# Performance work log

Hardware: AMD Instinct MI355X
Metric: run time of the kernel (lower is better)

## Reference

```python
import jax, jax.numpy as jnp
import numpy as np

B = 16384          # flattened rollout batch (T*N)
F = 512            # bc_args['features_dim']
H = 256            # hidden_size
E = 8              # num_skills
OUT = 32           # dim_action * steps_action = 8 * 4
DIM_ACTION = 8     # bc_args['dim_action'] + 1; output truncated to this


def setup_inputs() -> dict:
    key = jax.random.key(0)
    ks = jax.random.split(key, 5)
    features = jax.random.normal(ks[0], (B, F), dtype=jnp.float32)
    # expert MLP params, stacked over the E skills; fan-in scaled init
    W1 = jax.random.normal(ks[1], (E, F, H), dtype=jnp.float32) / np.sqrt(F)
    b1 = jnp.zeros((E, H), dtype=jnp.float32)
    W2 = jax.random.normal(ks[2], (E, H, H), dtype=jnp.float32) / np.sqrt(H)
    b2 = jnp.zeros((E, H), dtype=jnp.float32)
    W3 = jax.random.normal(ks[3], (E, H, OUT), dtype=jnp.float32) / np.sqrt(H)
    b3 = jnp.zeros((E, OUT), dtype=jnp.float32)
    master_action = jax.random.randint(ks[4], (B,), 0, E, dtype=jnp.int64)
    return {"features": features, "W1": W1, "b1": b1, "W2": W2, "b2": b2,
            "W3": W3, "b3": b3, "master_action": master_action}


def reference(features, W1, b1, W2, b2, W3, b3, master_action):
    # Per-sample skill dispatch: sample i goes through skills[master_action[i]],
    # a Linear->ReLU->Linear->ReLU->Linear MLP, output truncated to DIM_ACTION.
    # Vectorized as: run every expert over the full batch (E is a small fixed
    # set, so a Python loop over experts is fine), then select per-sample.
    sel = master_action[:, None]                      # [B, 1]
    out = jnp.zeros((features.shape[0], DIM_ACTION), dtype=features.dtype)
    for e in range(E):
        h = jax.nn.relu(features @ W1[e] + b1[e])     # [B, H]
        h = jax.nn.relu(h @ W2[e] + b2[e])            # [B, H]
        y = (h @ W3[e] + b3[e])[:, :DIM_ACTION]       # [B, DIM_ACTION]
        out = jnp.where(sel == e, y, out)
    return out
```

## Files before the change

### kernel.cpp

```cpp
#include <hip/hip_runtime.h>

#define B_TOTAL 16384
#define F_DIM 512
#define H_DIM 256
#define E_NUM 8
#define OUT_COLS 32
#define DA 8
#define TM 32
#define HSTRIDE (H_DIM + 8)

typedef __attribute__((ext_vector_type(8))) _Float16 half8;
typedef __attribute__((ext_vector_type(4))) _Float16 half4;
typedef __attribute__((ext_vector_type(4))) float float4v;

__global__ void k_bucket(const int* __restrict__ act, int* __restrict__ counts,
                         int* __restrict__ idxbuf) {
  __shared__ int wcnt[4][E_NUM];
  __shared__ int wbase[4][E_NUM];
  int t = threadIdx.x;
  int lane = t & 63, wave = t >> 6;
  int b = blockIdx.x * 256 + t;
  int e = act[b] & 7;

  unsigned long long mymask = 0;
#pragma unroll
  for (int v = 0; v < E_NUM; ++v) {
    unsigned long long m = __ballot(e == v);
    if (lane == 0) wcnt[wave][v] = (int)__popcll(m);
    if (e == v) mymask = m;
  }
  int rank = (int)__popcll(mymask & ((1ull << lane) - 1ull));
  __syncthreads();
  if (t < E_NUM) {
    int c0 = wcnt[0][t], c1 = wcnt[1][t], c2 = wcnt[2][t], c3 = wcnt[3][t];
    int base = atomicAdd(&counts[t], c0 + c1 + c2 + c3);
    wbase[0][t] = base;
    wbase[1][t] = base + c0;
    wbase[2][t] = base + c0 + c1;
    wbase[3][t] = base + c0 + c1 + c2;
  }
  __syncthreads();
  idxbuf[e * B_TOTAL + wbase[wave][e] + rank] = b;
}

__global__ void k_prep(const float* __restrict__ W1, const float* __restrict__ W2,
                       const float* __restrict__ W3,
                       _Float16* __restrict__ W1t, _Float16* __restrict__ W2t,
                       _Float16* __restrict__ W3t) {
  __shared__ float tile[32][33];
  int bid = blockIdx.x;
  int tx = threadIdx.x & 31, ty = threadIdx.x >> 5;

  const float* S; _Float16* D; int K, N, k0, n0;
  if (bid < 1024) {
    int e = bid >> 7, tt = bid & 127;
    K = F_DIM; N = H_DIM; k0 = (tt >> 3) * 32; n0 = (tt & 7) * 32;
    S = W1 + (size_t)e * F_DIM * H_DIM;
    D = W1t + (size_t)e * H_DIM * F_DIM;
  } else if (bid < 1536) {
    int r = bid - 1024;
    int e = r >> 6, tt = r & 63;
    K = H_DIM; N = H_DIM; k0 = (tt >> 3) * 32; n0 = (tt & 7) * 32;
    S = W2 + (size_t)e * H_DIM * H_DIM;
    D = W2t + (size_t)e * H_DIM * H_DIM;
  } else {
    int e = bid - 1536;
    int k = threadIdx.x;
#pragma unroll
    for (int o = 0; o < 16; ++o) {
      float v = (o < DA) ? W3[((size_t)e * H_DIM + k) * OUT_COLS + o] : 0.f;
      W3t[((size_t)e * 16 + o) * H_DIM + k] = (_Float16)v;
    }
    return;
  }
#pragma unroll
  for (int r = 0; r < 32; r += 8)
    tile[ty + r][tx] = S[(size_t)(k0 + ty + r) * N + (n0 + tx)];
  __syncthreads();
#pragma unroll
  for (int r = 0; r < 32; r += 8)
    D[(size_t)(n0 + ty + r) * K + (k0 + tx)] = (_Float16)tile[tx][ty + r];
}

__global__ void k_gather(const float* __restrict__ X, const int* __restrict__ counts,
                         const int* __restrict__ idxbuf, _Float16* __restrict__ Xg) {
  int wave = threadIdx.x >> 6, lane = threadIdx.x & 63;
  int slot = blockIdx.x * 4 + wave;

  int base = 0, e = -1, pos = 0, cnt_e = 0;
#pragma unroll
  for (int j = 0; j < E_NUM; ++j) {
    if (e < 0) {
      int c = counts[j];
      int rc = (c + 31) & ~31;
      if (slot < base + rc) { e = j; pos = slot - base; cnt_e = c; }
      else base += rc;
    }
  }
  if (e < 0) return;

  _Float16* dst = Xg + (size_t)slot * F_DIM + lane * 8;
  if (pos < cnt_e) {
    const float* src = X + (size_t)idxbuf[e * B_TOTAL + pos] * F_DIM + lane * 8;
    float4v x0 = *(const float4v*)src;
    float4v x1 = *(const float4v*)(src + 4);
    half8 h;
    h[0] = (_Float16)x0.x; h[1] = (_Float16)x0.y;
    h[2] = (_Float16)x0.z; h[3] = (_Float16)x0.w;
    h[4] = (_Float16)x1.x; h[5] = (_Float16)x1.y;
    h[6] = (_Float16)x1.z; h[7] = (_Float16)x1.w;
    *(half8*)dst = h;
  } else {
    half8 z = {};
    *(half8*)dst = z;
  }
}

__global__ __launch_bounds__(256, 3) void k_mlp(
    const _Float16* __restrict__ Xg,
    const _Float16* __restrict__ W1t,
    const _Float16* __restrict__ W2t,
    const _Float16* __restrict__ W3t,
    const float* __restrict__ b1,
    const float* __restrict__ b2,
    const float* __restrict__ b3,
    const int* __restrict__ counts,
    const int* __restrict__ idxbuf,
    float* __restrict__ out)
{
  int e = blockIdx.y;
  int cnt = counts[e];
  int tile0 = blockIdx.x * TM;
  if (tile0 >= cnt) return;

  int xbase = 0;
#pragma unroll
  for (int j = 0; j < E_NUM; ++j)
    if (j < e) xbase += (counts[j] + 31) & ~31;

  __shared__ _Float16 H1s[TM][HSTRIDE];
  __shared__ _Float16 H2s[TM][HSTRIDE];

  int t = threadIdx.x;
  int lane = t & 63;
  int wave = t >> 6;
  int quad = lane >> 4;
  int l16 = lane & 15;
  int hbase = wave * 64;
  int kq = quad * 8;

  const float4v vzero = {0.f, 0.f, 0.f, 0.f};
  float4v acc[4][2];
#pragma unroll
  for (int mt = 0; mt < 4; ++mt)
#pragma unroll
    for (int st = 0; st < 2; ++st) acc[mt][st] = vzero;

  {
    const _Float16* wb = W1t + ((size_t)e * H_DIM + hbase + l16) * F_DIM + kq;
    const _Float16* xb = Xg + ((size_t)(xbase + tile0) + l16) * F_DIM + kq;
    half8 a_p[2][4], b_p[2][2];
#pragma unroll
    for (int p = 0; p < 2; ++p) {
#pragma unroll
      for (int mt = 0; mt < 4; ++mt)
        a_p[p][mt] = *(const half8*)(wb + (size_t)mt * 16 * F_DIM + p * 32);
#pragma unroll
      for (int st = 0; st < 2; ++st)
        b_p[p][st] = *(const half8*)(xb + (size_t)st * 16 * F_DIM + p * 32);
    }
#pragma unroll
    for (int kb = 0; kb < F_DIM; kb += 32) {
      int p = (kb >> 5) & 1;
      half8 a_cur[4], b_cur[2];
#pragma unroll
      for (int mt = 0; mt < 4; ++mt) a_cur[mt] = a_p[p][mt];
#pragma unroll
      for (int st = 0; st < 2; ++st) b_cur[st] = b_p[p][st];
      if (kb + 64 < F_DIM) {
#pragma unroll
        for (int mt = 0; mt < 4; ++mt)
          a_p[p][mt] = *(const half8*)(wb + (size_t)mt * 16 * F_DIM + kb + 64);
#pragma unroll
        for (int st = 0; st < 2; ++st)
          b_p[p][st] = *(const half8*)(xb + (size_t)st * 16 * F_DIM + kb + 64);
      }
#pragma unroll
      for (int mt = 0; mt < 4; ++mt)
#pragma unroll
        for (int st = 0; st < 2; ++st)
          acc[mt][st] = __builtin_amdgcn_mfma_f32_16x16x32_f16(a_cur[mt], b_cur[st], acc[mt][st], 0, 0, 0);
    }
#pragma unroll
    for (int mt = 0; mt < 4; ++mt) {
      int h0 = hbase + mt * 16 + quad * 4;
      float4v bb = *(const float4v*)&b1[e * H_DIM + h0];
#pragma unroll
      for (int st = 0; st < 2; ++st) {
        half4 hv;
#pragma unroll
        for (int r = 0; r < 4; ++r) {
          float v = acc[mt][st][r] + bb[r];
          hv[r] = (_Float16)(v > 0.f ? v : 0.f);
        }
        *(half4*)&H1s[st * 16 + l16][h0] = hv;
      }
    }
  }
  __syncthreads();

#pragma unroll
  for (int mt = 0; mt < 4; ++mt)
#pragma unroll
    for (int st = 0; st < 2; ++st) acc[mt][st] = vzero;
  {
    const _Float16* wb = W2t + ((size_t)e * H_DIM + hbase + l16) * H_DIM + kq;
    half8 a_p[2][4];
#pragma unroll
    for (int p = 0; p < 2; ++p)
#pragma unroll
      for (int mt = 0; mt < 4; ++mt)
        a_p[p][mt] = *(const half8*)(wb + (size_t)mt * 16 * H_DIM + p * 32);
#pragma unroll
    for (int kb = 0; kb < H_DIM; kb += 32) {
      int p = (kb >> 5) & 1;
      half8 a_cur[4];
#pragma unroll
      for (int mt = 0; mt < 4; ++mt) a_cur[mt] = a_p[p][mt];
      if (kb + 64 < H_DIM) {
#pragma unroll
        for (int mt = 0; mt < 4; ++mt)
          a_p[p][mt] = *(const half8*)(wb + (size_t)mt * 16 * H_DIM + kb + 64);
      }
      half8 b_cur[2];
#pragma unroll
      for (int st = 0; st < 2; ++st)
        b_cur[st] = *(const half8*)&H1s[st * 16 + l16][kb + kq];
#pragma unroll
      for (int mt = 0; mt < 4; ++mt)
#pragma unroll
        for (int st = 0; st < 2; ++st)
          acc[mt][st] = __builtin_amdgcn_mfma_f32_16x16x32_f16(a_cur[mt], b_cur[st], acc[mt][st], 0, 0, 0);
    }
#pragma unroll
    for (int mt = 0; mt < 4; ++mt) {
      int h0 = hbase + mt * 16 + quad * 4;
      float4v bb = *(const float4v*)&b2[e * H_DIM + h0];
#pragma unroll
      for (int st = 0; st < 2; ++st) {
        half4 hv;
#pragma unroll
        for (int r = 0; r < 4; ++r) {
          float v = acc[mt][st][r] + bb[r];
          hv[r] = (_Float16)(v > 0.f ? v : 0.f);
        }
        *(half4*)&H2s[st * 16 + l16][h0] = hv;
      }
    }
  }
  __syncthreads();

  if (wave < 2) {
    float4v acc3 = vzero;
    const _Float16* wb = W3t + ((size_t)e * 16 + l16) * H_DIM + kq;
#pragma unroll
    for (int kb = 0; kb < H_DIM; kb += 32) {
      half8 afrag = *(const half8*)(wb + kb);
      half8 bfrag = *(const half8*)&H2s[wave * 16 + l16][kb + kq];
      acc3 = __builtin_amdgcn_mfma_f32_16x16x32_f16(afrag, bfrag, acc3, 0, 0, 0);
    }
    int si = tile0 + wave * 16 + l16;
    if (quad < 2 && si < cnt) {
      int row = idxbuf[e * B_TOTAL + si];
      float4v bb = *(const float4v*)&b3[e * OUT_COLS + quad * 4];
      float4v y;
#pragma unroll
      for (int r = 0; r < 4; ++r) y[r] = acc3[r] + bb[r];
      *(float4v*)&out[(size_t)row * DA + quad * 4] = y;
    }
  }
}

extern "C" void kernel_launch(void* const* d_in, const int* in_sizes, int n_in,
                              void* d_out, int out_size, void* d_ws, size_t ws_size,
                              hipStream_t stream) {
  const float* features = (const float*)d_in[0];
  const float* W1 = (const float*)d_in[1];
  const float* b1 = (const float*)d_in[2];
  const float* W2 = (const float*)d_in[3];
  const float* b2 = (const float*)d_in[4];
  const float* W3 = (const float*)d_in[5];
  const float* b3 = (const float*)d_in[6];
  const int* act = (const int*)d_in[7];
  float* out = (float*)d_out;

  char* ws = (char*)d_ws;
  int* counts = (int*)ws;
  int* idxbuf = (int*)(ws + 256);
  _Float16* W1t = (_Float16*)(ws + 256 + 524288);
  _Float16* W2t = (_Float16*)(ws + 256 + 524288 + 2097152);
  _Float16* W3t = (_Float16*)(ws + 256 + 524288 + 2097152 + 1048576);
  _Float16* Xg  = (_Float16*)(ws + 256 + 524288 + 2097152 + 1048576 + 65536);

  hipMemsetAsync(counts, 0, 256, stream);
  k_bucket<<<B_TOTAL / 256, 256, 0, stream>>>(act, counts, idxbuf);
  k_prep<<<1544, 256, 0, stream>>>(W1, W2, W3, W1t, W2t, W3t);
  k_gather<<<4160, 256, 0, stream>>>(features, counts, idxbuf, Xg);
  k_mlp<<<dim3(B_TOTAL / TM, E_NUM), 256, 0, stream>>>(Xg, W1t, W2t, W3t,
                                                       b1, b2, b3, counts, idxbuf, out);
}
```

Before: 143.3 us.

## Fuse bucketing into prep and gather features directly inside persistent MLP kernel

Bucketing of samples by skill moves into the weight-prep kernel, using per-block prefix scans instead of atomics, which removes the memset. The separate gather kernel and fp16 staging buffer are gone: the MLP kernel loads the indexed fp32 feature rows, converts them and stores them in LDS. The MLP kernel now runs a fixed grid of workers per expert looping over tiles, with H2 aliased onto the feature LDS buffer. This saves two launches and a global round trip, but adds a redundant prefix scan per bucketing block and exposes gather latency inside the MLP blocks.

```diff
diff --git a/kernel.cpp b/kernel.cpp
--- a/kernel.cpp
+++ b/kernel.cpp
@@ -7,117 +7,107 @@
 #define OUT_COLS 32
 #define DA 8
 #define TM 32
-#define HSTRIDE (H_DIM + 8)
+#define XSTRIDE 584
+#define HSTRIDE 280
 
 typedef __attribute__((ext_vector_type(8))) _Float16 half8;
 typedef __attribute__((ext_vector_type(4))) _Float16 half4;
 typedef __attribute__((ext_vector_type(4))) float float4v;
 
-__global__ void k_bucket(const int* __restrict__ act, int* __restrict__ counts,
-                         int* __restrict__ idxbuf) {
-  __shared__ int wcnt[4][E_NUM];
-  __shared__ int wbase[4][E_NUM];
+__global__ __launch_bounds__(256) void k_prep(
+    const float* __restrict__ W1, const float* __restrict__ W2,
+    const float* __restrict__ W3, const int* __restrict__ act,
+    _Float16* __restrict__ W1t, _Float16* __restrict__ W2t, _Float16* __restrict__ W3t,
+    int* __restrict__ idxbuf, int* __restrict__ counts)
+{
+  __shared__ float tile[32][33];
+  __shared__ int wavecnt[4][E_NUM];
+  __shared__ int wavepre[4][E_NUM];
+  __shared__ int pre[E_NUM];
+
+  int bid = blockIdx.x;
   int t = threadIdx.x;
   int lane = t & 63, wave = t >> 6;
-  int b = blockIdx.x * 256 + t;
-  int e = act[b] & 7;
-
-  unsigned long long mymask = 0;
-#pragma unroll
-  for (int v = 0; v < E_NUM; ++v) {
-    unsigned long long m = __ballot(e == v);
-    if (lane == 0) wcnt[wave][v] = (int)__popcll(m);
-    if (e == v) mymask = m;
+
+  if (bid < 64) {
+    int pcnt[E_NUM];
+#pragma unroll
+    for (int e = 0; e < E_NUM; ++e) pcnt[e] = 0;
+    for (int c = wave; c < bid; c += 4) {
+#pragma unroll
+      for (int s = 0; s < 4; ++s) {
+        int v = act[c * 256 + s * 64 + lane] & 7;
+#pragma unroll
+        for (int e = 0; e < E_NUM; ++e) {
+          unsigned long long m = __ballot(v == e);
+          pcnt[e] += (int)__popcll(m);
+        }
+      }
+    }
+    if (lane == 0)
+#pragma unroll
+      for (int e = 0; e < E_NUM; ++e) wavepre[wave][e] = pcnt[e];
+
+    int myB = bid * 256 + t;
+    int myE = act[myB] & 7;
+    unsigned long long mymask = 0;
+#pragma unroll
+    for (int v = 0; v < E_NUM; ++v) {
+      unsigned long long m = __ballot(myE == v);
+      if (lane == 0) wavecnt[wave][v] = (int)__popcll(m);
+      if (myE == v) mymask = m;
+    }
+    int rank = (int)__popcll(mymask & ((1ull << lane) - 1ull));
+    __syncthreads();
+    if (t < E_NUM)
+      pre[t] = wavepre[0][t] + wavepre[1][t] + wavepre[2][t] + wavepre[3][t];
+    __syncthreads();
+    int woff = 0;
+#pragma unroll
+    for (int w = 0; w < 3; ++w)
+      if (w < wave) woff += wavecnt[w][myE];
+    idxbuf[myE * B_TOTAL + pre[myE] + woff + rank] = myB;
+    if (bid == 63 && t < E_NUM)
+      counts[t] = pre[t] + wavecnt[0][t] + wavecnt[1][t] + wavecnt[2][t] + wavecnt[3][t];
+    return;
   }
-  int rank = (int)__popcll(mymask & ((1ull << lane) - 1ull));
-  __syncthreads();
-  if (t < E_NUM) {
-    int c0 = wcnt[0][t], c1 = wcnt[1][t], c2 = wcnt[2][t], c3 = wcnt[3][t];
-    int base = atomicAdd(&counts[t], c0 + c1 + c2 + c3);
-    wbase[0][t] = base;
-    wbase[1][t] = base + c0;
-    wbase[2][t] = base + c0 + c1;
-    wbase[3][t] = base + c0 + c1 + c2;
-  }
-  __syncthreads();
-  idxbuf[e * B_TOTAL + wbase[wave][e] + rank] = b;
-}
-
-__global__ void k_prep(const float* __restrict__ W1, const float* __restrict__ W2,
-                       const float* __restrict__ W3,
-                       _Float16* __restrict__ W1t, _Float16* __restrict__ W2t,
-                       _Float16* __restrict__ W3t) {
-  __shared__ float tile[32][33];
-  int bid = blockIdx.x;
-  int tx = threadIdx.x & 31, ty = threadIdx.x >> 5;
-
-  const float* S; _Float16* D; int K, N, k0, n0;
-  if (bid < 1024) {
-    int e = bid >> 7, tt = bid & 127;
-    K = F_DIM; N = H_DIM; k0 = (tt >> 3) * 32; n0 = (tt & 7) * 32;
-    S = W1 + (size_t)e * F_DIM * H_DIM;
-    D = W1t + (size_t)e * H_DIM * F_DIM;
-  } else if (bid < 1536) {
-    int r = bid - 1024;
-    int e = r >> 6, tt = r & 63;
-    K = H_DIM; N = H_DIM; k0 = (tt >> 3) * 32; n0 = (tt & 7) * 32;
-    S = W2 + (size_t)e * H_DIM * H_DIM;
-    D = W2t + (size_t)e * H_DIM * H_DIM;
+
+  int task = bid - 64;
+  int e = task & 7;
+  int sub = task >> 3;
+  int tx = t & 31, ty = t >> 5;
+
+  if (sub < 192) {
+    const float* S; _Float16* D; int K, N, k0, n0;
+    if (sub < 128) {
+      K = F_DIM; N = H_DIM; k0 = (sub >> 3) * 32; n0 = (sub & 7) * 32;
+      S = W1 + (size_t)e * F_DIM * H_DIM;
+      D = W1t + (size_t)e * H_DIM * F_DIM;
+    } else {
+      int s2 = sub - 128;
+      K = H_DIM; N = H_DIM; k0 = (s2 >> 3) * 32; n0 = (s2 & 7) * 32;
+      S = W2 + (size_t)e * H_DIM * H_DIM;
+      D = W2t + (size_t)e * H_DIM * H_DIM;
+    }
+#pragma unroll
+    for (int r = 0; r < 32; r += 8)
+      tile[ty + r][tx] = S[(size_t)(k0 + ty + r) * N + (n0 + tx)];
+    __syncthreads();
+#pragma unroll
+    for (int r = 0; r < 32; r += 8)
+      D[(size_t)(n0 + ty + r) * K + (k0 + tx)] = (_Float16)tile[tx][ty + r];
   } else {
-    int e = bid - 1536;
-    int k = threadIdx.x;
+    int k = t;
 #pragma unroll
     for (int o = 0; o < 16; ++o) {
       float v = (o < DA) ? W3[((size_t)e * H_DIM + k) * OUT_COLS + o] : 0.f;
       W3t[((size_t)e * 16 + o) * H_DIM + k] = (_Float16)v;
     }
-    return;
-  }
-#pragma unroll
-  for (int r = 0; r < 32; r += 8)
-    tile[ty + r][tx] = S[(size_t)(k0 + ty + r) * N + (n0 + tx)];
-  __syncthreads();
-#pragma unroll
-  for (int r = 0; r < 32; r += 8)
-    D[(size_t)(n0 + ty + r) * K + (k0 + tx)] = (_Float16)tile[tx][ty + r];
-}
-
-__global__ void k_gather(const float* __restrict__ X, const int* __restrict__ counts,
-                         const int* __restrict__ idxbuf, _Float16* __restrict__ Xg) {
-  int wave = threadIdx.x >> 6, lane = threadIdx.x & 63;
-  int slot = blockIdx.x * 4 + wave;
-
-  int base = 0, e = -1, pos = 0, cnt_e = 0;
-#pragma unroll
-  for (int j = 0; j < E_NUM; ++j) {
-    if (e < 0) {
-      int c = counts[j];
-      int rc = (c + 31) & ~31;
-      if (slot < base + rc) { e = j; pos = slot - base; cnt_e = c; }
-      else base += rc;
-    }
-  }
-  if (e < 0) return;
-
-  _Float16* dst = Xg + (size_t)slot * F_DIM + lane * 8;
-  if (pos < cnt_e) {
-    const float* src = X + (size_t)idxbuf[e * B_TOTAL + pos] * F_DIM + lane * 8;
-    float4v x0 = *(const float4v*)src;
-    float4v x1 = *(const float4v*)(src + 4);
-    half8 h;
-    h[0] = (_Float16)x0.x; h[1] = (_Float16)x0.y;
-    h[2] = (_Float16)x0.z; h[3] = (_Float16)x0.w;
-    h[4] = (_Float16)x1.x; h[5] = (_Float16)x1.y;
-    h[6] = (_Float16)x1.z; h[7] = (_Float16)x1.w;
-    *(half8*)dst = h;
-  } else {
-    half8 z = {};
-    *(half8*)dst = z;
   }
 }
 
-__global__ __launch_bounds__(256, 3) void k_mlp(
-    const _Float16* __restrict__ Xg,
+__global__ __launch_bounds__(256, 2) void k_mlp(
+    const float* __restrict__ X,
     const _Float16* __restrict__ W1t,
     const _Float16* __restrict__ W2t,
     const _Float16* __restrict__ W3t,
@@ -128,155 +118,172 @@
     const int* __restrict__ idxbuf,
     float* __restrict__ out)
 {
-  int e = blockIdx.y;
+  int e = blockIdx.x & 7;
+  int worker = blockIdx.x >> 3;
   int cnt = counts[e];
-  int tile0 = blockIdx.x * TM;
-  if (tile0 >= cnt) return;
-
-  int xbase = 0;
-#pragma unroll
-  for (int j = 0; j < E_NUM; ++j)
-    if (j < e) xbase += (counts[j] + 31) & ~31;
-
+  if (cnt <= 0) return;
+  int ntile = (cnt + TM - 1) / TM;
+
+  __shared__ _Float16 Xls[TM][XSTRIDE];
   __shared__ _Float16 H1s[TM][HSTRIDE];
-  __shared__ _Float16 H2s[TM][HSTRIDE];
+  __shared__ int idxg[TM];
+  _Float16 (*H2s)[HSTRIDE] = (_Float16(*)[HSTRIDE])&Xls[0][0];
 
   int t = threadIdx.x;
   int lane = t & 63;
   int wave = t >> 6;
   int quad = lane >> 4;
   int l16 = lane & 15;
+  int kq = quad * 8;
   int hbase = wave * 64;
-  int kq = quad * 8;
-
   const float4v vzero = {0.f, 0.f, 0.f, 0.f};
-  float4v acc[4][2];
-#pragma unroll
-  for (int mt = 0; mt < 4; ++mt)
-#pragma unroll
-    for (int st = 0; st < 2; ++st) acc[mt][st] = vzero;
-
-  {
-    const _Float16* wb = W1t + ((size_t)e * H_DIM + hbase + l16) * F_DIM + kq;
-    const _Float16* xb = Xg + ((size_t)(xbase + tile0) + l16) * F_DIM + kq;
-    half8 a_p[2][4], b_p[2][2];
-#pragma unroll
-    for (int p = 0; p < 2; ++p) {
-#pragma unroll
-      for (int mt = 0; mt < 4; ++mt)
-        a_p[p][mt] = *(const half8*)(wb + (size_t)mt * 16 * F_DIM + p * 32);
-#pragma unroll
-      for (int st = 0; st < 2; ++st)
-        b_p[p][st] = *(const half8*)(xb + (size_t)st * 16 * F_DIM + p * 32);
-    }
-#pragma unroll
-    for (int kb = 0; kb < F_DIM; kb += 32) {
-      int p = (kb >> 5) & 1;
-      half8 a_cur[4], b_cur[2];
-#pragma unroll
-      for (int mt = 0; mt < 4; ++mt) a_cur[mt] = a_p[p][mt];
-#pragma unroll
-      for (int st = 0; st < 2; ++st) b_cur[st] = b_p[p][st];
-      if (kb + 64 < F_DIM) {
+
+  for (int tile = worker; tile < ntile; tile += 64) {
+    int tile0 = tile * TM;
+    __syncthreads();
+    if (t < TM) {
+      int si = tile0 + t;
+      idxg[t] = idxbuf[e * B_TOTAL + (si < cnt ? si : cnt - 1)];
+    }
+    __syncthreads();
+
+#pragma unroll
+    for (int i = 0; i < 16; ++i) {
+      int c = i * 256 + t;
+      int row = c >> 7;
+      int col = (c & 127) * 4;
+      const float* src = X + (size_t)idxg[row] * F_DIM + col;
+      float4v x = *(const float4v*)src;
+      half4 h;
+      h[0] = (_Float16)x.x; h[1] = (_Float16)x.y;
+      h[2] = (_Float16)x.z; h[3] = (_Float16)x.w;
+      *(half4*)&Xls[row][col] = h;
+    }
+    __syncthreads();
+
+    float4v acc[4][2];
+#pragma unroll
+    for (int mt = 0; mt < 4; ++mt)
+#pragma unroll
+      for (int st = 0; st < 2; ++st) acc[mt][st] = vzero;
+
+    {
+      const _Float16* wb = W1t + ((size_t)e * H_DIM + hbase + l16) * F_DIM + kq;
+      half8 a_p[2][4];
+#pragma unroll
+      for (int p = 0; p < 2; ++p)
 #pragma unroll
         for (int mt = 0; mt < 4; ++mt)
-          a_p[p][mt] = *(const half8*)(wb + (size_t)mt * 16 * F_DIM + kb + 64);
+          a_p[p][mt] = *(const half8*)(wb + (size_t)mt * 16 * F_DIM + p * 32);
+#pragma unroll
+      for (int kb = 0; kb < F_DIM; kb += 32) {
+        int p = (kb >> 5) & 1;
+        half8 a_cur[4];
+#pragma unroll
+        for (int mt = 0; mt < 4; ++mt) a_cur[mt] = a_p[p][mt];
+        if (kb + 64 < F_DIM) {
+#pragma unroll
+          for (int mt = 0; mt < 4; ++mt)
+            a_p[p][mt] = *(const half8*)(wb + (size_t)mt * 16 * F_DIM + kb + 64);
+        }
+        half8 b_cur[2];
 #pragma unroll
         for (int st = 0; st < 2; ++st)
-          b_p[p][st] = *(const half8*)(xb + (size_t)st * 16 * F_DIM + kb + 64);
-      }
-#pragma unroll
-      for (int mt = 0; mt < 4; ++mt)
+          b_cur[st] = *(const half8*)&Xls[st * 16 + l16][kb + kq];
+#pragma unroll
+        for (int mt = 0; mt < 4; ++mt)
+#pragma unroll
+          for (int st = 0; st < 2; ++st)
+            acc[mt][st] = __builtin_amdgcn_mfma_f32_16x16x32_f16(a_cur[mt], b_cur[st], acc[mt][st], 0, 0, 0);
+      }
+#pragma unroll
+      for (int mt = 0; mt < 4; ++mt) {
+        int h0 = hbase + mt * 16 + quad * 4;
+        float4v bb = *(const float4v*)&b1[e * H_DIM + h0];
+#pragma unroll
+        for (int st = 0; st < 2; ++st) {
+          half4 hv;
+#pragma unroll
+          for (int r = 0; r < 4; ++r) {
+            float v = acc[mt][st][r] + bb[r];
+            hv[r] = (_Float16)(v > 0.f ? v : 0.f);
+          }
+          *(half4*)&H1s[st * 16 + l16][h0] = hv;
+        }
+      }
+    }
+    __syncthreads();
+
+#pragma unroll
+    for (int mt = 0; mt < 4; ++mt)
+#pragma unroll
+      for (int st = 0; st < 2; ++st) acc[mt][st] = vzero;
+    {
+      const _Float16* wb = W2t + ((size_t)e * H_DIM + hbase + l16) * H_DIM + kq;
+      half8 a_p[2][4];
+#pragma unroll
+      for (int p = 0; p < 2; ++p)
+#pragma unroll
+        for (int mt = 0; mt < 4; ++mt)
+          a_p[p][mt] = *(const half8*)(wb + (size_t)mt * 16 * H_DIM + p * 32);
+#pragma unroll
+      for (int kb = 0; kb < H_DIM; kb += 32) {
+        int p = (kb >> 5) & 1;
+        half8 a_cur[4];
+#pragma unroll
+        for (int mt = 0; mt < 4; ++mt) a_cur[mt] = a_p[p][mt];
+        if (kb + 64 < H_DIM) {
+#pragma unroll
+          for (int mt = 0; mt < 4; ++mt)
+            a_p[p][mt] = *(const half8*)(wb + (size_t)mt * 16 * H_DIM + kb + 64);
+        }
+        half8 b_cur[2];
 #pragma unroll
         for (int st = 0; st < 2; ++st)
-          acc[mt][st] = __builtin_amdgcn_mfma_f32_16x16x32_f16(a_cur[mt], b_cur[st], acc[mt][st], 0, 0, 0);
-    }
-#pragma unroll
-    for (int mt = 0; mt < 4; ++mt) {
-      int h0 = hbase + mt * 16 + quad * 4;
-      float4v bb = *(const float4v*)&b1[e * H_DIM + h0];
-#pragma unroll
-      for (int st = 0; st < 2; ++st) {
-        half4 hv;
-#pragma unroll
-        for (int r = 0; r < 4; ++r) {
-          float v = acc[mt][st][r] + bb[r];
-          hv[r] = (_Float16)(v > 0.f ? v : 0.f);
-        }
-        *(half4*)&H1s[st * 16 + l16][h0] = hv;
-      }
-    }
-  }
-  __syncthreads();
-
-#pragma unroll
-  for (int mt = 0; mt < 4; ++mt)
-#pragma unroll
-    for (int st = 0; st < 2; ++st) acc[mt][st] = vzero;
-  {
-    const _Float16* wb = W2t + ((size_t)e * H_DIM + hbase + l16) * H_DIM + kq;
-    half8 a_p[2][4];
-#pragma unroll
-    for (int p = 0; p < 2; ++p)
-#pragma unroll
-      for (int mt = 0; mt < 4; ++mt)
-        a_p[p][mt] = *(const half8*)(wb + (size_t)mt * 16 * H_DIM + p * 32);
-#pragma unroll
-    for (int kb = 0; kb < H_DIM; kb += 32) {
-      int p = (kb >> 5) & 1;
-      half8 a_cur[4];
-#pragma unroll
-      for (int mt = 0; mt < 4; ++mt) a_cur[mt] = a_p[p][mt];
-      if (kb + 64 < H_DIM) {
+          b_cur[st] = *(const half8*)&H1s[st * 16 + l16][kb + kq];
 #pragma unroll
         for (int mt = 0; mt < 4; ++mt)
-          a_p[p][mt] = *(const half8*)(wb + (size_t)mt * 16 * H_DIM + kb + 64);
-      }
-      half8 b_cur[2];
-#pragma unroll
-      for (int st = 0; st < 2; ++st)
-        b_cur[st] = *(const half8*)&H1s[st * 16 + l16][kb + kq];
-#pragma unroll
-      for (int mt = 0; mt < 4; ++mt)
-#pragma unroll
-        for (int st = 0; st < 2; ++st)
-          acc[mt][st] = __builtin_amdgcn_mfma_f32_16x16x32_f16(a_cur[mt], b_cur[st], acc[mt][st], 0, 0, 0);
-    }
-#pragma unroll
-    for (int mt = 0; mt < 4; ++mt) {
-      int h0 = hbase + mt * 16 + quad * 4;
-      float4v bb = *(const float4v*)&b2[e * H_DIM + h0];
-#pragma unroll
-      for (int st = 0; st < 2; ++st) {
-        half4 hv;
-#pragma unroll
-        for (int r = 0; r < 4; ++r) {
-          float v = acc[mt][st][r] + bb[r];
-          hv[r] = (_Float16)(v > 0.f ? v : 0.f);
-        }
-        *(half4*)&H2s[st * 16 + l16][h0] = hv;
-      }
-    }
-  }
-  __syncthreads();
-
-  if (wave < 2) {
-    float4v acc3 = vzero;
-    const _Float16* wb = W3t + ((size_t)e * 16 + l16) * H_DIM + kq;
-#pragma unroll
-    for (int kb = 0; kb < H_DIM; kb += 32) {
-      half8 afrag = *(const half8*)(wb + kb);
-      half8 bfrag = *(const half8*)&H2s[wave * 16 + l16][kb + kq];
-      acc3 = __builtin_amdgcn_mfma_f32_16x16x32_f16(afrag, bfrag, acc3, 0, 0, 0);
-    }
-    int si = tile0 + wave * 16 + l16;
-    if (quad < 2 && si < cnt) {
-      int row = idxbuf[e * B_TOTAL + si];
-      float4v bb = *(const float4v*)&b3[e * OUT_COLS + quad * 4];
-      float4v y;
-#pragma unroll
-      for (int r = 0; r < 4; ++r) y[r] = acc3[r] + bb[r];
-      *(float4v*)&out[(size_t)row * DA + quad * 4] = y;
+#pragma unroll
+          for (int st = 0; st < 2; ++st)
+            acc[mt][st] = __builtin_amdgcn_mfma_f32_16x16x32_f16(a_cur[mt], b_cur[st], acc[mt][st], 0, 0, 0);
+      }
+      __syncthreads();
+#pragma unroll
+      for (int mt = 0; mt < 4; ++mt) {
+        int h0 = hbase + mt * 16 + quad * 4;
+        float4v bb = *(const float4v*)&b2[e * H_DIM + h0];
+#pragma unroll
+        for (int st = 0; st < 2; ++st) {
+          half4 hv;
+#pragma unroll
+          for (int r = 0; r < 4; ++r) {
+            float v = acc[mt][st][r] + bb[r];
+            hv[r] = (_Float16)(v > 0.f ? v : 0.f);
+          }
+          *(half4*)&H2s[st * 16 + l16][h0] = hv;
+        }
+      }
+    }
+    __syncthreads();
+
+    if (wave < 2) {
+      float4v acc3 = vzero;
+      const _Float16* wb3 = W3t + ((size_t)e * 16 + l16) * H_DIM + kq;
+#pragma unroll
+      for (int kb = 0; kb < H_DIM; kb += 32) {
+        half8 afrag = *(const half8*)(wb3 + kb);
+        half8 bfrag = *(const half8*)&H2s[wave * 16 + l16][kb + kq];
+        acc3 = __builtin_amdgcn_mfma_f32_16x16x32_f16(afrag, bfrag, acc3, 0, 0, 0);
+      }
+      int si = tile0 + wave * 16 + l16;
+      if (quad < 2 && si < cnt) {
+        int row = idxg[wave * 16 + l16];
+        float4v bb = *(const float4v*)&b3[e * OUT_COLS + quad * 4];
+        float4v y;
+#pragma unroll
+        for (int r = 0; r < 4; ++r) y[r] = acc3[r] + bb[r];
+        *(float4v*)&out[(size_t)row * DA + quad * 4] = y;
+      }
     }
   }
 }
@@ -300,12 +307,7 @@
   _Float16* W1t = (_Float16*)(ws + 256 + 524288);
   _Float16* W2t = (_Float16*)(ws + 256 + 524288 + 2097152);
   _Float16* W3t = (_Float16*)(ws + 256 + 524288 + 2097152 + 1048576);
-  _Float16* Xg  = (_Float16*)(ws + 256 + 524288 + 2097152 + 1048576 + 65536);
-
-  hipMemsetAsync(counts, 0, 256, stream);
-  k_bucket<<<B_TOTAL / 256, 256, 0, stream>>>(act, counts, idxbuf);
-  k_prep<<<1544, 256, 0, stream>>>(W1, W2, W3, W1t, W2t, W3t);
-  k_gather<<<4160, 256, 0, stream>>>(features, counts, idxbuf, Xg);
-  k_mlp<<<dim3(B_TOTAL / TM, E_NUM), 256, 0, stream>>>(Xg, W1t, W2t, W3t,
-                                                       b1, b2, b3, counts, idxbuf, out);
+
+  k_prep<<<64 + 8 * 193, 256, 0, stream>>>(W1, W2, W3, act, W1t, W2t, W3t, idxbuf, counts);
+  k_mlp<<<512, 256, 0, stream>>>(features, W1t, W2t, W3t, b1, b2, b3, counts, idxbuf, out);
 }
```

After: 180.6 us. 1.26x slower.
